# Kernel tuning notes

Measured on AMD Instinct MI355X. Metric: run time of the kernel, lower is better.

Reference implementation:

```python
import jax, jax.numpy as jnp
import numpy as np

N_NODES = 100000
N_EDGES = 1200000
HIDDEN = 64
EDGE_DIM = 16
LN_EPS = 1e-6  # flax LayerNorm default


def setup_inputs() -> dict:
    key = jax.random.key(0)
    ks = jax.random.split(key, 10)
    node_features = jax.random.normal(ks[0], (N_NODES, HIDDEN), dtype=jnp.float32)
    edge_index = jax.random.randint(ks[1], (2, N_EDGES), 0, N_NODES, dtype=jnp.int64)
    edge_features = jax.random.normal(ks[2], (N_EDGES, EDGE_DIM), dtype=jnp.float32)
    # Dense(hidden) on concat([src_feat, edge_features]) -> in = HIDDEN+EDGE_DIM
    s1 = 1.0 / np.sqrt(HIDDEN + EDGE_DIM)
    W1 = jax.random.normal(ks[3], (HIDDEN + EDGE_DIM, HIDDEN), dtype=jnp.float32) * s1
    b1 = jnp.zeros((HIDDEN,), dtype=jnp.float32)
    s2 = 1.0 / np.sqrt(HIDDEN)
    W2 = jax.random.normal(ks[4], (HIDDEN, HIDDEN), dtype=jnp.float32) * s2
    b2 = jnp.zeros((HIDDEN,), dtype=jnp.float32)
    # update Dense on concat([node_features, agg]) -> in = 2*HIDDEN
    s3 = 1.0 / np.sqrt(2 * HIDDEN)
    W3 = jax.random.normal(ks[5], (2 * HIDDEN, HIDDEN), dtype=jnp.float32) * s3
    b3 = jnp.zeros((HIDDEN,), dtype=jnp.float32)
    ln_scale = jnp.ones((HIDDEN,), dtype=jnp.float32)
    ln_bias = jnp.zeros((HIDDEN,), dtype=jnp.float32)
    return {
        "node_features": node_features,
        "edge_features": edge_features,
        "edge_index": edge_index,
        "W1": W1, "b1": b1, "W2": W2, "b2": b2,
        "W3": W3, "b3": b3,
        "ln_scale": ln_scale, "ln_bias": ln_bias,
    }


def reference(node_features, edge_features, edge_index, W1, b1, W2, b2, W3, b3, ln_scale, ln_bias):
    # eval mode: dropout is identity (deterministic)
    src, dst = edge_index[0], edge_index[1]
    src_feat = node_features[src]                                  # [E, H] gather
    msg = jnp.concatenate([src_feat, edge_features], axis=-1)      # [E, H+Fe]
    msg = jax.nn.gelu(msg @ W1 + b1)                               # [E, H]
    msg = msg @ W2 + b2                                            # [E, H]
    agg = jax.ops.segment_sum(msg, dst, num_segments=node_features.shape[0])  # [N, H]
    upd = jnp.concatenate([node_features, agg], axis=-1)           # [N, 2H]
    h = upd @ W3 + b3                                              # [N, H]
    # LayerNorm (flax default: eps=1e-6, with scale and bias)
    mu = jnp.mean(h, axis=-1, keepdims=True)
    var = jnp.mean(jnp.square(h - mu), axis=-1, keepdims=True)
    h = (h - mu) * jax.lax.rsqrt(var + LN_EPS) * ln_scale + ln_bias
    h = jax.nn.gelu(h)
    # residual (node feature dim == hidden_dim)
    return h + node_features
```

## Files before the change

kernel.cpp:

```cpp
#include <hip/hip_runtime.h>

#define TE 64
#define TN 64

union F4 { float4 v; float f[4]; };

__device__ __forceinline__ float gelu_f(float x) {
    const float c0 = 0.7978845608028654f;
    float z = c0 * (x + 0.044715f * x * x * x);
    float ez = __builtin_exp2f(z * 2.8853900817779268f);
    float th = 1.0f - 2.0f * __builtin_amdgcn_rcpf(ez + 1.0f);
    return 0.5f * x * (1.0f + th);
}

__device__ __forceinline__ void barrier_lgkm() {
    asm volatile("s_waitcnt lgkmcnt(0)" ::: "memory");
    __builtin_amdgcn_s_barrier();
}

__global__ __launch_bounds__(256, 6) void edge_np_kernel(
    const float* __restrict__ ef,
    const int4*  __restrict__ esd,
    const float* __restrict__ np,
    const float* __restrict__ W1,
    const float* __restrict__ b1,
    float*       __restrict__ gsum,
    int nE, int nTiles)
{
    __shared__ float sX[16][TE + 4];
    __shared__ float sM[64][TE + 4];
    __shared__ int   sDst[TE];
    __shared__ int   sSrc[TE];

    const int t    = threadIdx.x;
    const int lane = t & 63;
    const int w    = t >> 6;
    const int e0   = (t & 15) * 4;
    const int c0   = (t >> 4) * 4;
    F4 b1v;
    b1v.v = *(const float4*)(b1 + c0);

    for (int tile = blockIdx.x; tile < nTiles; tile += gridDim.x) {
        const int gbase = tile * TE;
        {
            const int idx = gbase + lane;
            const int ci  = idx < nE ? idx : nE - 1;
            const int4 e  = esd[ci];
            F4 ev;
            ev.v = *(const float4*)(ef + (size_t)e.z * 16 + w * 4);
            #pragma unroll
            for (int j = 0; j < 4; ++j)
                sX[w * 4 + j][lane] = ev.f[j];
            if (w == 0) sDst[lane] = (idx < nE) ? e.y : -1;
            if (w == 1) sSrc[lane] = e.x;
        }
        barrier_lgkm();

        float acc[4][4] = {};
        #pragma unroll
        for (int k = 0; k < 16; ++k) {
            F4 xv, wv;
            xv.v = *(const float4*)&sX[k][e0];
            wv.v = *(const float4*)(W1 + (64 + k) * 64 + c0);
            #pragma unroll
            for (int i = 0; i < 4; ++i)
                #pragma unroll
                for (int j = 0; j < 4; ++j)
                    acc[i][j] = fmaf(xv.f[i], wv.f[j], acc[i][j]);
        }
        #pragma unroll
        for (int i = 0; i < 4; ++i) {
            F4 npv;
            npv.v = *(const float4*)(np + (size_t)sSrc[e0 + i] * 64 + c0);
            #pragma unroll
            for (int j = 0; j < 4; ++j)
                acc[i][j] += npv.f[j];
        }

        #pragma unroll
        for (int j = 0; j < 4; ++j) {
            F4 col;
            #pragma unroll
            for (int i = 0; i < 4; ++i)
                col.f[i] = gelu_f(acc[i][j] + b1v.f[j]);
            *(float4*)&sM[c0 + j][e0] = col.v;
        }
        barrier_lgkm();

        const int c  = t >> 2;
        const int q  = t & 3;
        const int cb = q * 16;
        int   cur = -1;
        float run = 0.f;
        #pragma unroll
        for (int s = 0; s < 4; ++s) {
            F4 rv;
            rv.v = *(const float4*)&sM[c][cb + s * 4];
            #pragma unroll
            for (int j = 0; j < 4; ++j) {
                const int d = sDst[cb + s * 4 + j];
                if (d != cur) {
                    if (cur >= 0)
                        __hip_atomic_fetch_add(gsum + (size_t)cur * 64 + c, run,
                                               __ATOMIC_RELAXED, __HIP_MEMORY_SCOPE_AGENT);
                    cur = d;
                    run = 0.f;
                }
                if (d >= 0) run += rv.f[j];
            }
        }
        if (cur >= 0)
            __hip_atomic_fetch_add(gsum + (size_t)cur * 64 + c, run,
                                   __ATOMIC_RELAXED, __HIP_MEMORY_SCOPE_AGENT);
        barrier_lgkm();
    }
}

__global__ __launch_bounds__(256, 4) void edge_mlp_kernel(
    const float* __restrict__ nf, const float* __restrict__ ef,
    const int* __restrict__ ei,
    const float* __restrict__ W1, const float* __restrict__ b1,
    const float* __restrict__ W2, const float* __restrict__ b2,
    float* agg, int nE, int nTiles)
{
    __shared__ float sX[80][TE + 4];
    __shared__ float sM[64][TE + 4];
    __shared__ int   sDst[TE];

    const int t    = threadIdx.x;
    const int lane = t & 63;
    const int w    = t >> 6;
    const int e0   = (t & 15) * 4;
    const int c0   = (t >> 4) * 4;
    F4 b1v, b2v;
    b1v.v = *(const float4*)(b1 + c0);
    b2v.v = *(const float4*)(b2 + c0);

    for (int tile = blockIdx.x; tile < nTiles; tile += gridDim.x) {
        const int gbase = tile * TE;
        {
            const int idx = gbase + lane;
            const int ge  = idx < nE ? idx : nE - 1;
            const int src = ei[ge];
            const int dstv = (idx < nE) ? ei[nE + ge] : -1;
            const float4* nrow = (const float4*)(nf + (size_t)src * 64);
            F4 a0, a1, a2, a3, ev;
            a0.v = nrow[w * 4 + 0];
            a1.v = nrow[w * 4 + 1];
            a2.v = nrow[w * 4 + 2];
            a3.v = nrow[w * 4 + 3];
            ev.v = *(const float4*)(ef + (size_t)ge * 16 + w * 4);
            const int kb = w * 16;
            #pragma unroll
            for (int j = 0; j < 4; ++j) {
                sX[kb + 0  + j][lane] = a0.f[j];
                sX[kb + 4  + j][lane] = a1.f[j];
                sX[kb + 8  + j][lane] = a2.f[j];
                sX[kb + 12 + j][lane] = a3.f[j];
                sX[64 + w * 4 + j][lane] = ev.f[j];
            }
            if (w == 0) sDst[lane] = dstv;
        }
        barrier_lgkm();

        float acc[4][4] = {};
        #pragma unroll 8
        for (int k = 0; k < 80; ++k) {
            F4 xv, wv;
            xv.v = *(const float4*)&sX[k][e0];
            wv.v = *(const float4*)(W1 + k * 64 + c0);
            #pragma unroll
            for (int i = 0; i < 4; ++i)
                #pragma unroll
                for (int j = 0; j < 4; ++j)
                    acc[i][j] = fmaf(xv.f[i], wv.f[j], acc[i][j]);
        }
        #pragma unroll
        for (int j = 0; j < 4; ++j) {
            F4 col;
            #pragma unroll
            for (int i = 0; i < 4; ++i)
                col.f[i] = gelu_f(acc[i][j] + b1v.f[j]);
            *(float4*)&sM[c0 + j][e0] = col.v;
        }
        barrier_lgkm();

        float acc2[4][4] = {};
        #pragma unroll 8
        for (int k = 0; k < 64; ++k) {
            F4 xv, wv;
            xv.v = *(const float4*)&sM[k][e0];
            wv.v = *(const float4*)(W2 + k * 64 + c0);
            #pragma unroll
            for (int i = 0; i < 4; ++i)
                #pragma unroll
                for (int j = 0; j < 4; ++j)
                    acc2[i][j] = fmaf(xv.f[i], wv.f[j], acc2[i][j]);
        }
        #pragma unroll
        for (int i = 0; i < 4; ++i) {
            if (gbase + e0 + i < nE) {
                float* arow = agg + (size_t)sDst[e0 + i] * 64 + c0;
                #pragma unroll
                for (int j = 0; j < 4; ++j)
                    __hip_atomic_fetch_add(arow + j, acc2[i][j] + b2v.f[j],
                                           __ATOMIC_RELAXED, __HIP_MEMORY_SCOPE_AGENT);
            }
        }
        barrier_lgkm();
    }
}

__global__ __launch_bounds__(256) void node_part_kernel(
    const float* __restrict__ nf, const float* __restrict__ W1,
    float* __restrict__ np, int nN)
{
    __shared__ float sU[64][TN + 4];
    const int t = threadIdx.x;
    const int lane = t & 63;
    const int w = t >> 6;
    const int tb = blockIdx.x * TN;
    const int node = (tb + lane < nN) ? tb + lane : nN - 1;
    {
        const float4* nrow = (const float4*)(nf + (size_t)node * 64);
        F4 a0, a1, a2, a3;
        a0.v = nrow[w * 4 + 0];
        a1.v = nrow[w * 4 + 1];
        a2.v = nrow[w * 4 + 2];
        a3.v = nrow[w * 4 + 3];
        const int kb = w * 16;
        #pragma unroll
        for (int j = 0; j < 4; ++j) {
            sU[kb + 0  + j][lane] = a0.f[j];
            sU[kb + 4  + j][lane] = a1.f[j];
            sU[kb + 8  + j][lane] = a2.f[j];
            sU[kb + 12 + j][lane] = a3.f[j];
        }
    }
    barrier_lgkm();
    const int n0 = (t & 15) * 4;
    const int c0 = (t >> 4) * 4;
    float acc[4][4] = {};
    #pragma unroll 8
    for (int k = 0; k < 64; ++k) {
        F4 xv, wv;
        xv.v = *(const float4*)&sU[k][n0];
        wv.v = *(const float4*)(W1 + k * 64 + c0);
        #pragma unroll
        for (int i = 0; i < 4; ++i)
            #pragma unroll
            for (int j = 0; j < 4; ++j)
                acc[i][j] = fmaf(xv.f[i], wv.f[j], acc[i][j]);
    }
    #pragma unroll
    for (int i = 0; i < 4; ++i) {
        const int gnode = tb + n0 + i;
        if (gnode < nN) {
            F4 o;
            #pragma unroll
            for (int j = 0; j < 4; ++j) o.f[j] = acc[i][j];
            *(float4*)(np + (size_t)gnode * 64 + c0) = o.v;
        }
    }
}

__global__ void prep_w23_kernel(const float* __restrict__ W2, const float* __restrict__ W3,
                                const float* __restrict__ b2,
                                float* __restrict__ W23, float* __restrict__ b2w)
{
    const int t = threadIdx.x;
    const int c = t & 63;
    const int kg = t >> 6;
    for (int k = kg * 16; k < kg * 16 + 16; ++k) {
        float s = 0.f;
        for (int m = 0; m < 64; ++m)
            s = fmaf(W2[k * 64 + m], W3[(64 + m) * 64 + c], s);
        W23[k * 64 + c] = s;
    }
    if (t < 64) {
        float s = 0.f;
        for (int m = 0; m < 64; ++m)
            s = fmaf(b2[m], W3[(64 + m) * 64 + t], s);
        b2w[t] = s;
    }
}

__global__ __launch_bounds__(256) void hist_kernel(const int* __restrict__ dst,
                                                   int* __restrict__ counts, int nE) {
    int e = blockIdx.x * 256 + threadIdx.x;
    const int stride = gridDim.x * 256;
    for (; e < nE; e += stride)
        atomicAdd(&counts[dst[e]], 1);
}

__global__ __launch_bounds__(256) void scan_local_kernel(const int* __restrict__ in,
                                                         int* __restrict__ out,
                                                         int* __restrict__ bsum, int n) {
    __shared__ int s[256];
    const int t = threadIdx.x;
    const int base = blockIdx.x * 2048 + t * 8;
    int v[8];
    #pragma unroll
    for (int i = 0; i < 8; ++i) v[i] = (base + i < n) ? in[base + i] : 0;
    int run = 0;
    #pragma unroll
    for (int i = 0; i < 8; ++i) { int c = v[i]; v[i] = run; run += c; }
    s[t] = run;
    __syncthreads();
    int x = run;
    for (int off = 1; off < 256; off <<= 1) {
        int y = (t >= off) ? s[t - off] : 0;
        __syncthreads();
        x += y; s[t] = x;
        __syncthreads();
    }
    const int texcl = x - run;
    if (t == 255) bsum[blockIdx.x] = x;
    #pragma unroll
    for (int i = 0; i < 8; ++i)
        if (base + i < n) out[base + i] = texcl + v[i];
}

__global__ void scan_bsums_kernel(int* bsum, int nb) {
    const int l = threadIdx.x;
    if (nb <= 64) {
        int v = (l < nb) ? bsum[l] : 0;
        const int orig = v;
        for (int off = 1; off < 64; off <<= 1) {
            int y = __shfl_up(v, off, 64);
            if (l >= off) v += y;
        }
        if (l < nb) bsum[l] = v - orig;
    } else if (l == 0) {
        int run = 0;
        for (int b = 0; b < nb; ++b) { int tt = bsum[b]; bsum[b] = run; run += tt; }
    }
}

__global__ __launch_bounds__(256) void scan_add_kernel(int* __restrict__ offs,
                                                       const int* __restrict__ bsum,
                                                       int* __restrict__ cursor, int n) {
    const int base = blockIdx.x * 2048 + threadIdx.x * 8;
    const int add = bsum[blockIdx.x];
    #pragma unroll
    for (int i = 0; i < 8; ++i)
        if (base + i < n) { int v = offs[base + i] + add; offs[base + i] = v; cursor[base + i] = v; }
}

__global__ __launch_bounds__(256) void scatter_kernel(const int* __restrict__ ei,
                                                      int* __restrict__ cursor,
                                                      int4* __restrict__ esd, int nE) {
    int e = blockIdx.x * 256 + threadIdx.x;
    const int stride = gridDim.x * 256;
    for (; e < nE; e += stride) {
        const int s = ei[e];
        const int d = ei[nE + e];
        const int pos = atomicAdd(&cursor[d], 1);
        esd[pos] = make_int4(s, d, e, 0);
    }
}

__global__ __launch_bounds__(256) void node_update_kernel(
    const float* __restrict__ nf,
    const float* gsum,
    const float* __restrict__ W3,
    const float* __restrict__ wB,
    const float* __restrict__ b3,
    const float* __restrict__ cvec,
    const int*   __restrict__ counts,
    const float* __restrict__ lns,
    const float* __restrict__ lnb,
    float* out, int nN)
{
    __shared__ float sW3[128][64];
    __shared__ float sU[128][TN + 4];
    __shared__ float sP1[16][TN];
    __shared__ float sP2[16][TN];
    __shared__ float sMu[TN];
    __shared__ float sRs[TN];

    const int t = threadIdx.x;
    for (int i = t * 4; i < 64 * 64; i += 1024)
        *(float4*)((float*)sW3 + i) = *(const float4*)(W3 + i);
    for (int i = t * 4; i < 64 * 64; i += 1024)
        *(float4*)((float*)sW3 + 4096 + i) = *(const float4*)(wB + i);

    const int lane = t & 63;
    const int w    = t >> 6;
    const int tb   = blockIdx.x * TN;
    const int node = tb + lane;
    const bool valid = node < nN;

    {
        const float* base = (w < 2) ? (nf   + (size_t)node * 64 + w * 32)
                                    : (gsum + (size_t)node * 64 + (w - 2) * 32);
        const int kb = (w < 2) ? (w * 32) : (64 + (w - 2) * 32);
        #pragma unroll
        for (int q = 0; q < 8; ++q) {
            F4 v;
            v.v = valid ? *(const float4*)(base + q * 4) : make_float4(0.f, 0.f, 0.f, 0.f);
            #pragma unroll
            for (int j = 0; j < 4; ++j)
                sU[kb + q * 4 + j][lane] = v.f[j];
        }
    }

    const int n0 = (t & 15) * 4;
    const int c0 = (t >> 4) * 4;
    F4 b3v, sv, bv, cv;
    b3v.v = *(const float4*)(b3  + c0);
    sv.v  = *(const float4*)(lns + c0);
    bv.v  = *(const float4*)(lnb + c0);
    if (cvec) cv.v = *(const float4*)(cvec + c0);
    __syncthreads();

    float acc[4][4] = {};
    #pragma unroll 8
    for (int k = 0; k < 128; ++k) {
        F4 xv, wv;
        xv.v = *(const float4*)&sU[k][n0];
        wv.v = *(const float4*)&sW3[k][c0];
        #pragma unroll
        for (int i = 0; i < 4; ++i)
            #pragma unroll
            for (int j = 0; j < 4; ++j)
                acc[i][j] = fmaf(xv.f[i], wv.f[j], acc[i][j]);
    }

    float h[4][4];
    #pragma unroll
    for (int i = 0; i < 4; ++i) {
        float cf = 0.f;
        if (counts) {
            const int gnode = tb + n0 + i;
            cf = (float)counts[gnode < nN ? gnode : nN - 1];
        }
        #pragma unroll
        for (int j = 0; j < 4; ++j) {
            float v = acc[i][j] + b3v.f[j];
            if (cvec) v = fmaf(cf, cv.f[j], v);
            h[i][j] = v;
        }
    }

    const int cg = t >> 4;
    #pragma unroll
    for (int i = 0; i < 4; ++i) {
        float s1 = h[i][0] + h[i][1] + h[i][2] + h[i][3];
        float s2 = h[i][0]*h[i][0] + h[i][1]*h[i][1] + h[i][2]*h[i][2] + h[i][3]*h[i][3];
        sP1[cg][n0 + i] = s1;
        sP2[cg][n0 + i] = s2;
    }
    __syncthreads();
    if (t < TN) {
        float m1 = 0.f, m2 = 0.f;
        #pragma unroll
        for (int g = 0; g < 16; ++g) { m1 += sP1[g][t]; m2 += sP2[g][t]; }
        float mu  = m1 * (1.f / 64.f);
        float var = m2 * (1.f / 64.f) - mu * mu;
        sMu[t] = mu;
        sRs[t] = rsqrtf(var + 1e-6f);
    }
    __syncthreads();

    #pragma unroll
    for (int i = 0; i < 4; ++i) {
        const int gnode = tb + n0 + i;
        const float mu = sMu[n0 + i];
        const float rs = sRs[n0 + i];
        if (gnode < nN) {
            #pragma unroll
            for (int j = 0; j < 4; ++j) {
                float xn = (h[i][j] - mu) * rs * sv.f[j] + bv.f[j];
                float r  = gelu_f(xn) + sU[c0 + j][n0 + i];
                out[(size_t)gnode * 64 + c0 + j] = r;
            }
        }
    }
}

extern "C" void kernel_launch(void* const* d_in, const int* in_sizes, int n_in,
                              void* d_out, int out_size, void* d_ws, size_t ws_size,
                              hipStream_t stream)
{
    const float* nf  = (const float*)d_in[0];
    const float* ef  = (const float*)d_in[1];
    const int*   ei  = (const int*)  d_in[2];
    const float* W1  = (const float*)d_in[3];
    const float* b1  = (const float*)d_in[4];
    const float* W2  = (const float*)d_in[5];
    const float* b2  = (const float*)d_in[6];
    const float* W3  = (const float*)d_in[7];
    const float* b3  = (const float*)d_in[8];
    const float* lns = (const float*)d_in[9];
    const float* lnb = (const float*)d_in[10];

    const int nN = in_sizes[0] / 64;
    const int nE = in_sizes[2] / 2;
    float* out = (float*)d_out;
    const int* dstArr = ei + nE;

    const int gridB = (nN + TN - 1) / TN;
    const int nTiles = (nE + TE - 1) / TE;

    char* ws = (char*)d_ws;
    size_t off = 0;
    auto take = [&](size_t bytes) { void* p = ws + off; off = (off + bytes + 255) & ~(size_t)255; return p; };
    int*   counts = (int*)  take((size_t)nN * 4);
    int*   offs   = (int*)  take((size_t)nN * 4);
    int*   cursor = (int*)  take((size_t)nN * 4);
    int*   bsum   = (int*)  take(4096);
    int4*  esd    = (int4*) take((size_t)nE * 16);
    float* W23    = (float*)take(64 * 64 * 4);
    float* b2w    = (float*)take(64 * 4);
    float* npart  = (float*)take((size_t)nN * 64 * 4);
    const size_t tier2End = off;
    float* gsumw  = (float*)take((size_t)nN * 64 * 4);
    const size_t tier3End = off;
    const size_t aggBytes = (size_t)nN * 64 * 4;

    if (ws_size >= tier2End) {
        float* gsum = (ws_size >= tier3End) ? gsumw : out;
        const int nb = (nN + 2047) / 2048;
        hipMemsetAsync(counts, 0, (size_t)nN * 4, stream);
        hipMemsetAsync(gsum, 0, aggBytes, stream);
        hipLaunchKernelGGL(hist_kernel, dim3(2048), dim3(256), 0, stream, dstArr, counts, nE);
        hipLaunchKernelGGL(scan_local_kernel, dim3(nb), dim3(256), 0, stream, counts, offs, bsum, nN);
        hipLaunchKernelGGL(scan_bsums_kernel, dim3(1), dim3(64), 0, stream, bsum, nb);
        hipLaunchKernelGGL(scan_add_kernel, dim3(nb), dim3(256), 0, stream, offs, bsum, cursor, nN);
        hipLaunchKernelGGL(scatter_kernel, dim3(2048), dim3(256), 0, stream, ei, cursor, esd, nE);
        hipLaunchKernelGGL(prep_w23_kernel, dim3(1), dim3(256), 0, stream, W2, W3, b2, W23, b2w);
        hipLaunchKernelGGL(node_part_kernel, dim3(gridB), dim3(256), 0, stream, nf, W1, npart, nN);

        const int gridE = nTiles < 1536 ? nTiles : 1536;
        hipLaunchKernelGGL(edge_np_kernel, dim3(gridE), dim3(256), 0, stream,
                           ef, esd, npart, W1, b1, gsum, nE, nTiles);

        hipLaunchKernelGGL(node_update_kernel, dim3(gridB), dim3(256), 0, stream,
                           nf, gsum, W3, W23, b3, b2w, counts, lns, lnb, out, nN);
    } else {
        const int gridA = nTiles < 1024 ? nTiles : 1024;
        float* agg = (ws_size >= aggBytes) ? (float*)d_ws : out;
        hipMemsetAsync(agg, 0, aggBytes, stream);
        hipLaunchKernelGGL(edge_mlp_kernel, dim3(gridA), dim3(256), 0, stream,
                           nf, ef, ei, W1, b1, W2, b2, agg, nE, nTiles);
        hipLaunchKernelGGL(node_update_kernel, dim3(gridB), dim3(256), 0, stream,
                           nf, agg, W3, W3 + 64 * 64, b3, (const float*)nullptr, (const int*)nullptr,
                           lns, lnb, out, nN);
    }
}
```

Baseline: 413.0 us.

## Fuse memset and W23 prep into other kernels, prefetch src rows early

Removes the gsum memset by zeroing the accumulation buffer inside node_part_kernel, and merges the W23/b2w precompute into the bsum-scan kernel as a second block, cutting launch count. In the edge kernel, each thread loads its src indices directly from global memory and issues the npart row gathers before the edge-feature staging barrier, so gather latency overlaps the first matmul. Occupancy hint is raised from 6 to 7 and the persistent grid from 1536 to 1792. Risks include more register pressure from holding prefetched rows, and redundant index loads.

```diff
diff --git a/kernel.cpp b/kernel.cpp
--- a/kernel.cpp
+++ b/kernel.cpp
@@ -18,7 +18,7 @@
     __builtin_amdgcn_s_barrier();
 }
 
-__global__ __launch_bounds__(256, 6) void edge_np_kernel(
+__global__ __launch_bounds__(256, 7) void edge_np_kernel(
     const float* __restrict__ ef,
     const int4*  __restrict__ esd,
     const float* __restrict__ np,
@@ -30,18 +30,31 @@
     __shared__ float sX[16][TE + 4];
     __shared__ float sM[64][TE + 4];
     __shared__ int   sDst[TE];
-    __shared__ int   sSrc[TE];
 
     const int t    = threadIdx.x;
     const int lane = t & 63;
     const int w    = t >> 6;
     const int e0   = (t & 15) * 4;
     const int c0   = (t >> 4) * 4;
+    const int* esdInt = (const int*)esd;
     F4 b1v;
     b1v.v = *(const float4*)(b1 + c0);
 
     for (int tile = blockIdx.x; tile < nTiles; tile += gridDim.x) {
         const int gbase = tile * TE;
+
+        int srcs[4];
+        #pragma unroll
+        for (int i = 0; i < 4; ++i) {
+            int idx = gbase + e0 + i;
+            if (idx >= nE) idx = nE - 1;
+            srcs[i] = esdInt[(size_t)idx * 4];
+        }
+        F4 npv[4];
+        #pragma unroll
+        for (int i = 0; i < 4; ++i)
+            npv[i].v = *(const float4*)(np + (size_t)srcs[i] * 64 + c0);
+
         {
             const int idx = gbase + lane;
             const int ci  = idx < nE ? idx : nE - 1;
@@ -52,7 +65,6 @@
             for (int j = 0; j < 4; ++j)
                 sX[w * 4 + j][lane] = ev.f[j];
             if (w == 0) sDst[lane] = (idx < nE) ? e.y : -1;
-            if (w == 1) sSrc[lane] = e.x;
         }
         barrier_lgkm();
 
@@ -69,13 +81,10 @@
                     acc[i][j] = fmaf(xv.f[i], wv.f[j], acc[i][j]);
         }
         #pragma unroll
-        for (int i = 0; i < 4; ++i) {
-            F4 npv;
-            npv.v = *(const float4*)(np + (size_t)sSrc[e0 + i] * 64 + c0);
+        for (int i = 0; i < 4; ++i)
             #pragma unroll
             for (int j = 0; j < 4; ++j)
-                acc[i][j] += npv.f[j];
-        }
+                acc[i][j] += npv[i].f[j];
 
         #pragma unroll
         for (int j = 0; j < 4; ++j) {
@@ -213,7 +222,7 @@
 
 __global__ __launch_bounds__(256) void node_part_kernel(
     const float* __restrict__ nf, const float* __restrict__ W1,
-    float* __restrict__ np, int nN)
+    float* __restrict__ np, float* __restrict__ gz, int nN)
 {
     __shared__ float sU[64][TN + 4];
     const int t = threadIdx.x;
@@ -221,6 +230,15 @@
     const int w = t >> 6;
     const int tb = blockIdx.x * TN;
     const int node = (tb + lane < nN) ? tb + lane : nN - 1;
+    {
+        const float4 z = make_float4(0.f, 0.f, 0.f, 0.f);
+        const int base = tb * 64 + t * 4;
+        #pragma unroll
+        for (int p = 0; p < 4; ++p) {
+            const int idx = base + p * 1024;
+            if (idx < nN * 64) *(float4*)(gz + idx) = z;
+        }
+    }
     {
         const float4* nrow = (const float4*)(nf + (size_t)node * 64);
         F4 a0, a1, a2, a3;
@@ -264,24 +282,43 @@
     }
 }
 
-__global__ void prep_w23_kernel(const float* __restrict__ W2, const float* __restrict__ W3,
-                                const float* __restrict__ b2,
-                                float* __restrict__ W23, float* __restrict__ b2w)
+__global__ void scan_bsums_w23_kernel(int* bsum, int nb,
+                                      const float* __restrict__ W2, const float* __restrict__ W3,
+                                      const float* __restrict__ b2,
+                                      float* __restrict__ W23, float* __restrict__ b2w)
 {
     const int t = threadIdx.x;
-    const int c = t & 63;
-    const int kg = t >> 6;
-    for (int k = kg * 16; k < kg * 16 + 16; ++k) {
-        float s = 0.f;
-        for (int m = 0; m < 64; ++m)
-            s = fmaf(W2[k * 64 + m], W3[(64 + m) * 64 + c], s);
-        W23[k * 64 + c] = s;
-    }
-    if (t < 64) {
-        float s = 0.f;
-        for (int m = 0; m < 64; ++m)
-            s = fmaf(b2[m], W3[(64 + m) * 64 + t], s);
-        b2w[t] = s;
+    if (blockIdx.x == 0) {
+        if (t < 64) {
+            const int l = t;
+            if (nb <= 64) {
+                int v = (l < nb) ? bsum[l] : 0;
+                const int orig = v;
+                for (int off = 1; off < 64; off <<= 1) {
+                    int y = __shfl_up(v, off, 64);
+                    if (l >= off) v += y;
+                }
+                if (l < nb) bsum[l] = v - orig;
+            } else if (l == 0) {
+                int run = 0;
+                for (int b = 0; b < nb; ++b) { int tt = bsum[b]; bsum[b] = run; run += tt; }
+            }
+        }
+    } else {
+        const int c = t & 63;
+        const int kg = t >> 6;
+        for (int k = kg * 16; k < kg * 16 + 16; ++k) {
+            float s = 0.f;
+            for (int m = 0; m < 64; ++m)
+                s = fmaf(W2[k * 64 + m], W3[(64 + m) * 64 + c], s);
+            W23[k * 64 + c] = s;
+        }
+        if (t < 64) {
+            float s = 0.f;
+            for (int m = 0; m < 64; ++m)
+                s = fmaf(b2[m], W3[(64 + m) * 64 + t], s);
+            b2w[t] = s;
+        }
     }
 }
 
@@ -319,22 +356,6 @@
     #pragma unroll
     for (int i = 0; i < 8; ++i)
         if (base + i < n) out[base + i] = texcl + v[i];
-}
-
-__global__ void scan_bsums_kernel(int* bsum, int nb) {
-    const int l = threadIdx.x;
-    if (nb <= 64) {
-        int v = (l < nb) ? bsum[l] : 0;
-        const int orig = v;
-        for (int off = 1; off < 64; off <<= 1) {
-            int y = __shfl_up(v, off, 64);
-            if (l >= off) v += y;
-        }
-        if (l < nb) bsum[l] = v - orig;
-    } else if (l == 0) {
-        int run = 0;
-        for (int b = 0; b < nb; ++b) { int tt = bsum[b]; bsum[b] = run; run += tt; }
-    }
 }
 
 __global__ __launch_bounds__(256) void scan_add_kernel(int* __restrict__ offs,
@@ -523,16 +544,15 @@
         float* gsum = (ws_size >= tier3End) ? gsumw : out;
         const int nb = (nN + 2047) / 2048;
         hipMemsetAsync(counts, 0, (size_t)nN * 4, stream);
-        hipMemsetAsync(gsum, 0, aggBytes, stream);
         hipLaunchKernelGGL(hist_kernel, dim3(2048), dim3(256), 0, stream, dstArr, counts, nE);
         hipLaunchKernelGGL(scan_local_kernel, dim3(nb), dim3(256), 0, stream, counts, offs, bsum, nN);
-        hipLaunchKernelGGL(scan_bsums_kernel, dim3(1), dim3(64), 0, stream, bsum, nb);
+        hipLaunchKernelGGL(scan_bsums_w23_kernel, dim3(2), dim3(256), 0, stream,
+                           bsum, nb, W2, W3, b2, W23, b2w);
         hipLaunchKernelGGL(scan_add_kernel, dim3(nb), dim3(256), 0, stream, offs, bsum, cursor, nN);
         hipLaunchKernelGGL(scatter_kernel, dim3(2048), dim3(256), 0, stream, ei, cursor, esd, nE);
-        hipLaunchKernelGGL(prep_w23_kernel, dim3(1), dim3(256), 0, stream, W2, W3, b2, W23, b2w);
-        hipLaunchKernelGGL(node_part_kernel, dim3(gridB), dim3(256), 0, stream, nf, W1, npart, nN);
-
-        const int gridE = nTiles < 1536 ? nTiles : 1536;
+        hipLaunchKernelGGL(node_part_kernel, dim3(gridB), dim3(256), 0, stream, nf, W1, npart, gsum, nN);
+
+        const int gridE = nTiles < 1792 ? nTiles : 1792;
         hipLaunchKernelGGL(edge_np_kernel, dim3(gridE), dim3(256), 0, stream,
                            ef, esd, npart, W1, b1, gsum, nE, nTiles);
 
```

Result: slower. 495.0 us (+19.8%).

## Fuse CSR build stages into one persistent kernel with software grid barriers

Applied to the files above, without the earlier changes.

Replaces the separate memset, histogram, scan, scan-add, scatter and W23 prep launches with one persistent 512-block kernel that uses atomic-based grid barriers between phases. The gsum zeroing moves into node_part_kernel. The aim is to cut launch gaps and the cost of small kernels. The grid barrier assumes all 512 blocks are resident at once, and the scatter now runs over only 512 blocks where it previously had 2048.

```diff
diff --git a/kernel.cpp b/kernel.cpp
--- a/kernel.cpp
+++ b/kernel.cpp
@@ -2,6 +2,7 @@
 
 #define TE 64
 #define TN 64
+#define CSR_BLOCKS 512
 
 union F4 { float4 v; float f[4]; };
 
@@ -16,6 +17,21 @@
 __device__ __forceinline__ void barrier_lgkm() {
     asm volatile("s_waitcnt lgkmcnt(0)" ::: "memory");
     __builtin_amdgcn_s_barrier();
+}
+
+__device__ __forceinline__ void grid_sync(int* bar, int idx, int nblocks) {
+    __syncthreads();
+    if (threadIdx.x == 0) {
+        __threadfence();
+        if (__hip_atomic_fetch_add(&bar[idx * 2], 1, __ATOMIC_ACQ_REL, __HIP_MEMORY_SCOPE_AGENT)
+            == nblocks - 1) {
+            __hip_atomic_store(&bar[idx * 2 + 1], 1, __ATOMIC_RELEASE, __HIP_MEMORY_SCOPE_AGENT);
+        } else {
+            while (!__hip_atomic_load(&bar[idx * 2 + 1], __ATOMIC_ACQUIRE, __HIP_MEMORY_SCOPE_AGENT))
+                __builtin_amdgcn_s_sleep(1);
+        }
+    }
+    __syncthreads();
 }
 
 __global__ __launch_bounds__(256, 6) void edge_np_kernel(
@@ -113,6 +129,166 @@
             __hip_atomic_fetch_add(gsum + (size_t)cur * 64 + c, run,
                                    __ATOMIC_RELAXED, __HIP_MEMORY_SCOPE_AGENT);
         barrier_lgkm();
+    }
+}
+
+__global__ __launch_bounds__(256) void csr_build_kernel(
+    const int* __restrict__ ei, int nE, int nN,
+    int* __restrict__ counts, int* __restrict__ offs, int* __restrict__ cursor,
+    int* __restrict__ bsum, int4* __restrict__ esd, int* bar,
+    const float* __restrict__ W2, const float* __restrict__ W3, const float* __restrict__ b2,
+    float* __restrict__ W23, float* __restrict__ b2w)
+{
+    __shared__ int s[256];
+    const int t = threadIdx.x, b = blockIdx.x, nb = gridDim.x;
+    const int gtid = b * 256 + t, gsz = nb * 256;
+    const int* dst = ei + nE;
+    const int nChunks = (nN + 2047) / 2048;
+
+    for (int i = gtid; i < nN; i += gsz) counts[i] = 0;
+    if (b == nb - 1) {
+        const int c = t & 63;
+        const int kg = t >> 6;
+        for (int k = kg * 16; k < kg * 16 + 16; ++k) {
+            float sacc = 0.f;
+            for (int m = 0; m < 64; ++m)
+                sacc = fmaf(W2[k * 64 + m], W3[(64 + m) * 64 + c], sacc);
+            W23[k * 64 + c] = sacc;
+        }
+        if (t < 64) {
+            float sacc = 0.f;
+            for (int m = 0; m < 64; ++m)
+                sacc = fmaf(b2[m], W3[(64 + m) * 64 + t], sacc);
+            b2w[t] = sacc;
+        }
+    }
+    grid_sync(bar, 0, nb);
+
+    for (int e = gtid; e < nE; e += gsz)
+        atomicAdd(&counts[dst[e]], 1);
+    grid_sync(bar, 1, nb);
+
+    for (int ch = b; ch < nChunks; ch += nb) {
+        const int base = ch * 2048 + t * 8;
+        int v[8];
+        #pragma unroll
+        for (int i = 0; i < 8; ++i) v[i] = (base + i < nN) ? counts[base + i] : 0;
+        int run = 0;
+        #pragma unroll
+        for (int i = 0; i < 8; ++i) { int c = v[i]; v[i] = run; run += c; }
+        s[t] = run;
+        __syncthreads();
+        int x = run;
+        for (int off = 1; off < 256; off <<= 1) {
+            int y = (t >= off) ? s[t - off] : 0;
+            __syncthreads();
+            x += y; s[t] = x;
+            __syncthreads();
+        }
+        const int texcl = x - run;
+        if (t == 255) bsum[ch] = x;
+        #pragma unroll
+        for (int i = 0; i < 8; ++i)
+            if (base + i < nN) offs[base + i] = texcl + v[i];
+        __syncthreads();
+    }
+    grid_sync(bar, 2, nb);
+
+    if (b == 0) {
+        if (nChunks <= 64) {
+            if (t < 64) {
+                const int l = t;
+                int v = (l < nChunks) ? bsum[l] : 0;
+                const int orig = v;
+                for (int off = 1; off < 64; off <<= 1) {
+                    int y = __shfl_up(v, off, 64);
+                    if (l >= off) v += y;
+                }
+                if (l < nChunks) bsum[l] = v - orig;
+            }
+        } else if (t == 0) {
+            int run = 0;
+            for (int c2 = 0; c2 < nChunks; ++c2) { int tt = bsum[c2]; bsum[c2] = run; run += tt; }
+        }
+    }
+    grid_sync(bar, 3, nb);
+
+    for (int ch = b; ch < nChunks; ch += nb) {
+        const int add = bsum[ch];
+        const int base = ch * 2048 + t * 8;
+        #pragma unroll
+        for (int i = 0; i < 8; ++i)
+            if (base + i < nN) { int v = offs[base + i] + add; offs[base + i] = v; cursor[base + i] = v; }
+    }
+    grid_sync(bar, 4, nb);
+
+    for (int e = gtid; e < nE; e += gsz) {
+        const int sv = ei[e];
+        const int d  = dst[e];
+        const int pos = atomicAdd(&cursor[d], 1);
+        esd[pos] = make_int4(sv, d, e, 0);
+    }
+}
+
+__global__ __launch_bounds__(256) void node_part_kernel(
+    const float* __restrict__ nf, const float* __restrict__ W1,
+    float* __restrict__ np, float* __restrict__ gz, int nN)
+{
+    __shared__ float sU[64][TN + 4];
+    const int t = threadIdx.x;
+    const int lane = t & 63;
+    const int w = t >> 6;
+    const int tb = blockIdx.x * TN;
+    const int node = (tb + lane < nN) ? tb + lane : nN - 1;
+    {
+        const float4 z = make_float4(0.f, 0.f, 0.f, 0.f);
+        const int base = tb * 64 + t * 4;
+        #pragma unroll
+        for (int pz = 0; pz < 4; ++pz) {
+            const int idx = base + pz * 1024;
+            if (idx < nN * 64) *(float4*)(gz + idx) = z;
+        }
+    }
+    {
+        const float4* nrow = (const float4*)(nf + (size_t)node * 64);
+        F4 a0, a1, a2, a3;
+        a0.v = nrow[w * 4 + 0];
+        a1.v = nrow[w * 4 + 1];
+        a2.v = nrow[w * 4 + 2];
+        a3.v = nrow[w * 4 + 3];
+        const int kb = w * 16;
+        #pragma unroll
+        for (int j = 0; j < 4; ++j) {
+            sU[kb + 0  + j][lane] = a0.f[j];
+            sU[kb + 4  + j][lane] = a1.f[j];
+            sU[kb + 8  + j][lane] = a2.f[j];
+            sU[kb + 12 + j][lane] = a3.f[j];
+        }
+    }
+    barrier_lgkm();
+    const int n0 = (t & 15) * 4;
+    const int c0 = (t >> 4) * 4;
+    float acc[4][4] = {};
+    #pragma unroll 8
+    for (int k = 0; k < 64; ++k) {
+        F4 xv, wv;
+        xv.v = *(const float4*)&sU[k][n0];
+        wv.v = *(const float4*)(W1 + k * 64 + c0);
+        #pragma unroll
+        for (int i = 0; i < 4; ++i)
+            #pragma unroll
+            for (int j = 0; j < 4; ++j)
+                acc[i][j] = fmaf(xv.f[i], wv.f[j], acc[i][j]);
+    }
+    #pragma unroll
+    for (int i = 0; i < 4; ++i) {
+        const int gnode = tb + n0 + i;
+        if (gnode < nN) {
+            F4 o;
+            #pragma unroll
+            for (int j = 0; j < 4; ++j) o.f[j] = acc[i][j];
+            *(float4*)(np + (size_t)gnode * 64 + c0) = o.v;
+        }
     }
 }
 
@@ -208,155 +384,6 @@
             }
         }
         barrier_lgkm();
-    }
-}
-
-__global__ __launch_bounds__(256) void node_part_kernel(
-    const float* __restrict__ nf, const float* __restrict__ W1,
-    float* __restrict__ np, int nN)
-{
-    __shared__ float sU[64][TN + 4];
-    const int t = threadIdx.x;
-    const int lane = t & 63;
-    const int w = t >> 6;
-    const int tb = blockIdx.x * TN;
-    const int node = (tb + lane < nN) ? tb + lane : nN - 1;
-    {
-        const float4* nrow = (const float4*)(nf + (size_t)node * 64);
-        F4 a0, a1, a2, a3;
-        a0.v = nrow[w * 4 + 0];
-        a1.v = nrow[w * 4 + 1];
-        a2.v = nrow[w * 4 + 2];
-        a3.v = nrow[w * 4 + 3];
-        const int kb = w * 16;
-        #pragma unroll
-        for (int j = 0; j < 4; ++j) {
-            sU[kb + 0  + j][lane] = a0.f[j];
-            sU[kb + 4  + j][lane] = a1.f[j];
-            sU[kb + 8  + j][lane] = a2.f[j];
-            sU[kb + 12 + j][lane] = a3.f[j];
-        }
-    }
-    barrier_lgkm();
-    const int n0 = (t & 15) * 4;
-    const int c0 = (t >> 4) * 4;
-    float acc[4][4] = {};
-    #pragma unroll 8
-    for (int k = 0; k < 64; ++k) {
-        F4 xv, wv;
-        xv.v = *(const float4*)&sU[k][n0];
-        wv.v = *(const float4*)(W1 + k * 64 + c0);
-        #pragma unroll
-        for (int i = 0; i < 4; ++i)
-            #pragma unroll
-            for (int j = 0; j < 4; ++j)
-                acc[i][j] = fmaf(xv.f[i], wv.f[j], acc[i][j]);
-    }
-    #pragma unroll
-    for (int i = 0; i < 4; ++i) {
-        const int gnode = tb + n0 + i;
-        if (gnode < nN) {
-            F4 o;
-            #pragma unroll
-            for (int j = 0; j < 4; ++j) o.f[j] = acc[i][j];
-            *(float4*)(np + (size_t)gnode * 64 + c0) = o.v;
-        }
-    }
-}
-
-__global__ void prep_w23_kernel(const float* __restrict__ W2, const float* __restrict__ W3,
-                                const float* __restrict__ b2,
-                                float* __restrict__ W23, float* __restrict__ b2w)
-{
-    const int t = threadIdx.x;
-    const int c = t & 63;
-    const int kg = t >> 6;
-    for (int k = kg * 16; k < kg * 16 + 16; ++k) {
-        float s = 0.f;
-        for (int m = 0; m < 64; ++m)
-            s = fmaf(W2[k * 64 + m], W3[(64 + m) * 64 + c], s);
-        W23[k * 64 + c] = s;
-    }
-    if (t < 64) {
-        float s = 0.f;
-        for (int m = 0; m < 64; ++m)
-            s = fmaf(b2[m], W3[(64 + m) * 64 + t], s);
-        b2w[t] = s;
-    }
-}
-
-__global__ __launch_bounds__(256) void hist_kernel(const int* __restrict__ dst,
-                                                   int* __restrict__ counts, int nE) {
-    int e = blockIdx.x * 256 + threadIdx.x;
-    const int stride = gridDim.x * 256;
-    for (; e < nE; e += stride)
-        atomicAdd(&counts[dst[e]], 1);
-}
-
-__global__ __launch_bounds__(256) void scan_local_kernel(const int* __restrict__ in,
-                                                         int* __restrict__ out,
-                                                         int* __restrict__ bsum, int n) {
-    __shared__ int s[256];
-    const int t = threadIdx.x;
-    const int base = blockIdx.x * 2048 + t * 8;
-    int v[8];
-    #pragma unroll
-    for (int i = 0; i < 8; ++i) v[i] = (base + i < n) ? in[base + i] : 0;
-    int run = 0;
-    #pragma unroll
-    for (int i = 0; i < 8; ++i) { int c = v[i]; v[i] = run; run += c; }
-    s[t] = run;
-    __syncthreads();
-    int x = run;
-    for (int off = 1; off < 256; off <<= 1) {
-        int y = (t >= off) ? s[t - off] : 0;
-        __syncthreads();
-        x += y; s[t] = x;
-        __syncthreads();
-    }
-    const int texcl = x - run;
-    if (t == 255) bsum[blockIdx.x] = x;
-    #pragma unroll
-    for (int i = 0; i < 8; ++i)
-        if (base + i < n) out[base + i] = texcl + v[i];
-}
-
-__global__ void scan_bsums_kernel(int* bsum, int nb) {
-    const int l = threadIdx.x;
-    if (nb <= 64) {
-        int v = (l < nb) ? bsum[l] : 0;
-        const int orig = v;
-        for (int off = 1; off < 64; off <<= 1) {
-            int y = __shfl_up(v, off, 64);
-            if (l >= off) v += y;
-        }
-        if (l < nb) bsum[l] = v - orig;
-    } else if (l == 0) {
-        int run = 0;
-        for (int b = 0; b < nb; ++b) { int tt = bsum[b]; bsum[b] = run; run += tt; }
-    }
-}
-
-__global__ __launch_bounds__(256) void scan_add_kernel(int* __restrict__ offs,
-                                                       const int* __restrict__ bsum,
-                                                       int* __restrict__ cursor, int n) {
-    const int base = blockIdx.x * 2048 + threadIdx.x * 8;
-    const int add = bsum[blockIdx.x];
-    #pragma unroll
-    for (int i = 0; i < 8; ++i)
-        if (base + i < n) { int v = offs[base + i] + add; offs[base + i] = v; cursor[base + i] = v; }
-}
-
-__global__ __launch_bounds__(256) void scatter_kernel(const int* __restrict__ ei,
-                                                      int* __restrict__ cursor,
-                                                      int4* __restrict__ esd, int nE) {
-    int e = blockIdx.x * 256 + threadIdx.x;
-    const int stride = gridDim.x * 256;
-    for (; e < nE; e += stride) {
-        const int s = ei[e];
-        const int d = ei[nE + e];
-        const int pos = atomicAdd(&cursor[d], 1);
-        esd[pos] = make_int4(s, d, e, 0);
     }
 }
 
@@ -498,7 +525,6 @@
     const int nN = in_sizes[0] / 64;
     const int nE = in_sizes[2] / 2;
     float* out = (float*)d_out;
-    const int* dstArr = ei + nE;
 
     const int gridB = (nN + TN - 1) / TN;
     const int nTiles = (nE + TE - 1) / TE;
@@ -510,6 +536,7 @@
     int*   offs   = (int*)  take((size_t)nN * 4);
     int*   cursor = (int*)  take((size_t)nN * 4);
     int*   bsum   = (int*)  take(4096);
+    int*   bar    = (int*)  take(256);
     int4*  esd    = (int4*) take((size_t)nE * 16);
     float* W23    = (float*)take(64 * 64 * 4);
     float* b2w    = (float*)take(64 * 4);
@@ -521,16 +548,12 @@
 
     if (ws_size >= tier2End) {
         float* gsum = (ws_size >= tier3End) ? gsumw : out;
-        const int nb = (nN + 2047) / 2048;
-        hipMemsetAsync(counts, 0, (size_t)nN * 4, stream);
-        hipMemsetAsync(gsum, 0, aggBytes, stream);
-        hipLaunchKernelGGL(hist_kernel, dim3(2048), dim3(256), 0, stream, dstArr, counts, nE);
-        hipLaunchKernelGGL(scan_local_kernel, dim3(nb), dim3(256), 0, stream, counts, offs, bsum, nN);
-        hipLaunchKernelGGL(scan_bsums_kernel, dim3(1), dim3(64), 0, stream, bsum, nb);
-        hipLaunchKernelGGL(scan_add_kernel, dim3(nb), dim3(256), 0, stream, offs, bsum, cursor, nN);
-        hipLaunchKernelGGL(scatter_kernel, dim3(2048), dim3(256), 0, stream, ei, cursor, esd, nE);
-        hipLaunchKernelGGL(prep_w23_kernel, dim3(1), dim3(256), 0, stream, W2, W3, b2, W23, b2w);
-        hipLaunchKernelGGL(node_part_kernel, dim3(gridB), dim3(256), 0, stream, nf, W1, npart, nN);
+        hipMemsetAsync(bar, 0, 256, stream);
+        hipLaunchKernelGGL(csr_build_kernel, dim3(CSR_BLOCKS), dim3(256), 0, stream,
+                           ei, nE, nN, counts, offs, cursor, bsum, esd, bar,
+                           W2, W3, b2, W23, b2w);
+        hipLaunchKernelGGL(node_part_kernel, dim3(gridB), dim3(256), 0, stream,
+                           nf, W1, npart, gsum, nN);
 
         const int gridE = nTiles < 1536 ? nTiles : 1536;
         hipLaunchKernelGGL(edge_np_kernel, dim3(gridE), dim3(256), 0, stream,
```

Result: slower. 880.5 us (+113.2%).
